# Performance work log

Measured on AMD Instinct MI355X. Metric: run time of the kernel, lower is better.

## Reference

```python
import jax, jax.numpy as jnp
import numpy as np

N_NODES = 20000
N_EDGES = 320000
IN_F = 256
OUT_F = 64
HEADS = 4
ALPHA = 0.1  # leaky_relu negative slope


def setup_inputs() -> dict:
    key = jax.random.key(0)
    ks = jax.random.split(key, 8)
    return {
        "input1": jax.random.normal(ks[0], (N_NODES, IN_F), jnp.float32),
        "input2": jax.random.normal(ks[1], (N_NODES, IN_F), jnp.float32),
        # per-head params: Ws maps source feats -> target_out, Wt maps target feats -> source_out
        "Ws": jax.random.normal(ks[2], (HEADS, IN_F, OUT_F), jnp.float32) * 0.06,
        "Wt": jax.random.normal(ks[3], (HEADS, IN_F, OUT_F), jnp.float32) * 0.06,
        "a1": jax.random.normal(ks[4], (HEADS, 2 * OUT_F), jnp.float32) * 0.1,
        "a2": jax.random.normal(ks[5], (HEADS, 2 * OUT_F), jnp.float32) * 0.1,
        # COO nonzeros of A_opt [n_target, n_source]
        "tgt_idx": jax.random.randint(ks[6], (N_EDGES,), 0, N_NODES),
        "src_idx": jax.random.randint(ks[7], (N_EDGES,), 0, N_NODES),
    }


def _segment_softmax(scores, seg, num_segments):
    m = jax.lax.stop_gradient(jax.ops.segment_max(scores, seg, num_segments=num_segments))
    w = jnp.exp(scores - m[seg])
    d = jax.ops.segment_sum(w, seg, num_segments=num_segments)
    d = jnp.where(d == 0, 1.0, d)
    return w / d[seg]


def _head(x1, x2, Ws, Wt, a1, a2, src, tgt, n_s, n_t):
    s = x1 @ Ws  # [n_s, OUT_F]  messages source -> target
    t = x2 @ Wt  # [n_t, OUT_F]  messages target -> source
    out = Ws.shape[1]
    # edge score e = leaky_relu(a^T [s_src || t_tgt]); split a to avoid edge-level concat
    e1 = jax.nn.leaky_relu((s @ a1[:out])[src] + (t @ a1[out:])[tgt], ALPHA)
    e2 = jax.nn.leaky_relu((s @ a2[:out])[src] + (t @ a2[out:])[tgt], ALPHA)
    alpha_ts = _segment_softmax(e1, tgt, n_t)  # softmax over sources per target
    alpha_st = _segment_softmax(e2, src, n_s)  # softmax over targets per source
    h_ts = jax.ops.segment_sum(alpha_ts[:, None] * s[src], tgt, num_segments=n_t)
    h_st = jax.ops.segment_sum(alpha_st[:, None] * t[tgt], src, num_segments=n_s)
    return jax.nn.elu(h_st), jax.nn.elu(h_ts)  # concat=True -> ELU per head


def reference(input1, input2, Ws, Wt, a1, a2, tgt_idx, src_idx):
    n_s, n_t = input1.shape[0], input2.shape[0]
    head_fn = jax.vmap(
        lambda W1, W2, v1, v2: _head(input1, input2, W1, W2, v1, v2, src_idx, tgt_idx, n_s, n_t)
    )
    h_st, h_ts = head_fn(Ws, Wt, a1, a2)  # each [H, n, OUT_F]
    h_st = jnp.transpose(h_st, (1, 0, 2)).reshape(n_s, -1)  # concat heads
    h_ts = jnp.transpose(h_ts, (1, 0, 2)).reshape(n_t, -1)
    return h_st, h_ts
```

## Files before the change

kernel.cpp:

```cpp
#include <hip/hip_runtime.h>
#include <math.h>

#define N_NODES 20000
#define N_EDGES 320000
#define IN_F 256
#define OUT_F 64
#define HEADS 4
#define NCOL 256
#define LRELU_ALPHA 0.1f
#define ELL_CAP 64

#define SCAT_X 313
#define GEMM_GB 157

typedef __attribute__((ext_vector_type(8))) short short8;
typedef __attribute__((ext_vector_type(4))) float floatx4;

__device__ __forceinline__ float lrelu(float x) {
    return x > 0.f ? x : LRELU_ALPHA * x;
}
__device__ __forceinline__ unsigned short f2bf(float f) {
    unsigned int u = __float_as_uint(f);
    u = (u + 0x7FFF + ((u >> 16) & 1)) >> 16;
    return (unsigned short)u;
}
__device__ __forceinline__ float bf2f(unsigned short u) {
    return __uint_as_float(((unsigned int)u) << 16);
}

__global__ __launch_bounds__(256) void prep_w_kernel(
    const float* __restrict__ Ws, const float* __restrict__ Wt,
    unsigned short* __restrict__ Wsb, unsigned short* __restrict__ Wtb,
    int* __restrict__ cnt)
{
    const int gid = blockIdx.x * 256 + threadIdx.x;

    for (int i = gid; i < 2 * N_NODES; i += 16384) cnt[i] = 0;

    const int mat = gid >> 13;
    const int r   = gid & 8191;
    const int kc  = r >> 8;
    const int c   = r & 255;
    const float* W    = mat ? Wt : Ws;
    unsigned short* O = mat ? Wtb : Wsb;
    const int h = c >> 6, j = c & 63;
    const int k0 = kc * 8;
    unsigned short v[8] __attribute__((aligned(16)));
#pragma unroll
    for (int i = 0; i < 8; ++i)
        v[i] = f2bf(W[(size_t)h * (IN_F * OUT_F) + (size_t)(k0 + i) * OUT_F + j]);
    *(uint4*)(O + (size_t)c * IN_F + k0) = *(const uint4*)v;
}

__global__ __launch_bounds__(512, 4) void hybrid_kernel(
    const float* __restrict__ A0, const unsigned short* __restrict__ Wb0,
    const float* __restrict__ A1, const unsigned short* __restrict__ Wb1,
    unsigned short* __restrict__ C0, unsigned short* __restrict__ C1,
    const float* __restrict__ a1, const float* __restrict__ a2,
    float* __restrict__ ss1, float* __restrict__ ss2,
    float* __restrict__ tt1, float* __restrict__ tt2,
    const int* __restrict__ src, const int* __restrict__ tgt,
    int* __restrict__ cnt_t, int* __restrict__ cnt_s,
    unsigned short* __restrict__ elist_t, unsigned short* __restrict__ elist_s)
{
    const int tid = threadIdx.x;

    __shared__ __align__(16) unsigned short Bl[128][264];

    if (blockIdx.x < SCAT_X) {
        const int e = ((int)blockIdx.y * SCAT_X + (int)blockIdx.x) * 512 + tid;
        if (e < N_EDGES) {
            const int s = src[e], t = tgt[e];
            const int p = atomicAdd(&cnt_t[t], 1);
            const int q = atomicAdd(&cnt_s[s], 1);
            if (p < ELL_CAP) elist_t[t * ELL_CAP + p] = (unsigned short)s;
            if (q < ELL_CAP) elist_s[s * ELL_CAP + q] = (unsigned short)t;
        }
        return;
    }

    const int gx   = blockIdx.x - SCAT_X;
    const int half = gx & 1;
    const int gb   = gx >> 1;
    const float* A           = (blockIdx.y == 0) ? A0 : A1;
    const unsigned short* Wb = (blockIdx.y == 0) ? Wb0 : Wb1;
    unsigned short* C        = (blockIdx.y == 0) ? C0 : C1;

    for (int i = tid; i < 4096; i += 512) {
        const int n  = i >> 5;
        const int kc = (i & 31) << 3;
        *(uint4*)&Bl[n][kc] = *(const uint4*)(Wb + (size_t)(half * 128 + n) * IN_F + kc);
    }
    __syncthreads();

    const int lane = tid & 63;
    const int w    = tid >> 6;
    const int quad = lane >> 4;
    const int l15  = lane & 15;
    const int g    = gb * 8 + w;
    if (g >= 1250) return;

    const float* arow = A + (size_t)(g * 16 + l15) * IN_F + quad * 8;

    float4 ua[8];
#pragma unroll
    for (int kk = 0; kk < 4; ++kk) {
        ua[2 * kk]     = *(const float4*)(arow + kk * 32);
        ua[2 * kk + 1] = *(const float4*)(arow + kk * 32 + 4);
    }
    short8 af[4];
#pragma unroll
    for (int kk = 0; kk < 4; ++kk) {
        short8 t;
        t[0] = (short)f2bf(ua[2 * kk].x);     t[1] = (short)f2bf(ua[2 * kk].y);
        t[2] = (short)f2bf(ua[2 * kk].z);     t[3] = (short)f2bf(ua[2 * kk].w);
        t[4] = (short)f2bf(ua[2 * kk + 1].x); t[5] = (short)f2bf(ua[2 * kk + 1].y);
        t[6] = (short)f2bf(ua[2 * kk + 1].z); t[7] = (short)f2bf(ua[2 * kk + 1].w);
        af[kk] = t;
    }

    float4 ub[8];
#pragma unroll
    for (int kk = 0; kk < 4; ++kk) {
        ub[2 * kk]     = *(const float4*)(arow + (kk + 4) * 32);
        ub[2 * kk + 1] = *(const float4*)(arow + (kk + 4) * 32 + 4);
    }

    floatx4 acc[8];
#pragma unroll
    for (int c = 0; c < 8; ++c) acc[c] = (floatx4){0.f, 0.f, 0.f, 0.f};

#pragma unroll
    for (int kk = 0; kk < 4; ++kk) {
#pragma unroll
        for (int c = 0; c < 8; ++c) {
            short8 bfrag = *(const short8*)&Bl[c * 16 + l15][kk * 32 + quad * 8];
            acc[c] = __builtin_amdgcn_mfma_f32_16x16x32_bf16(af[kk], bfrag, acc[c], 0, 0, 0);
        }
    }

#pragma unroll
    for (int kk = 0; kk < 4; ++kk) {
        short8 t;
        t[0] = (short)f2bf(ub[2 * kk].x);     t[1] = (short)f2bf(ub[2 * kk].y);
        t[2] = (short)f2bf(ub[2 * kk].z);     t[3] = (short)f2bf(ub[2 * kk].w);
        t[4] = (short)f2bf(ub[2 * kk + 1].x); t[5] = (short)f2bf(ub[2 * kk + 1].y);
        t[6] = (short)f2bf(ub[2 * kk + 1].z); t[7] = (short)f2bf(ub[2 * kk + 1].w);
        af[kk] = t;
    }
#pragma unroll
    for (int kk = 0; kk < 4; ++kk) {
#pragma unroll
        for (int c = 0; c < 8; ++c) {
            short8 bfrag = *(const short8*)&Bl[c * 16 + l15][(kk + 4) * 32 + quad * 8];
            acc[c] = __builtin_amdgcn_mfma_f32_16x16x32_bf16(af[kk], bfrag, acc[c], 0, 0, 0);
        }
    }

#pragma unroll
    for (int c = 0; c < 8; ++c) {
        const int col = half * 128 + c * 16 + l15;
#pragma unroll
        for (int r = 0; r < 4; ++r) {
            const int m = g * 16 + quad * 4 + r;
            C[(size_t)m * NCOL + col] = f2bf(acc[c][r]);
        }
    }

    const int off_aj = (blockIdx.y == 0) ? 0 : 64;
    float* o1 = (blockIdx.y == 0) ? ss1 : tt1;
    float* o2 = (blockIdx.y == 0) ? ss2 : tt2;

    float p1[2][4] = {{0.f,0.f,0.f,0.f},{0.f,0.f,0.f,0.f}};
    float p2[2][4] = {{0.f,0.f,0.f,0.f},{0.f,0.f,0.f,0.f}};
#pragma unroll
    for (int c = 0; c < 8; ++c) {
        const int hl = c >> 2;
        const int hh = half * 2 + hl;
        const int jj = (c & 3) * 16 + l15;
        const float w1 = a1[hh * 128 + off_aj + jj];
        const float w2 = a2[hh * 128 + off_aj + jj];
#pragma unroll
        for (int r = 0; r < 4; ++r) {
            p1[hl][r] += acc[c][r] * w1;
            p2[hl][r] += acc[c][r] * w2;
        }
    }
#pragma unroll
    for (int m = 1; m < 16; m <<= 1) {
#pragma unroll
        for (int hl = 0; hl < 2; ++hl)
#pragma unroll
            for (int r = 0; r < 4; ++r) {
                p1[hl][r] += __shfl_xor(p1[hl][r], m, 64);
                p2[hl][r] += __shfl_xor(p2[hl][r], m, 64);
            }
    }
    if (l15 == 0) {
#pragma unroll
        for (int r = 0; r < 4; ++r) {
            const int m = g * 16 + quad * 4 + r;
#pragma unroll
            for (int hl = 0; hl < 2; ++hl) {
                const int hh = half * 2 + hl;
                o1[m * HEADS + hh] = p1[hl][r];
                o2[m * HEADS + hh] = p2[hl][r];
            }
        }
    }
}

__global__ __launch_bounds__(256) void agg_kernel(
    const int* __restrict__ cnt_t, const unsigned short* __restrict__ elist_t,
    const int* __restrict__ cnt_s, const unsigned short* __restrict__ elist_s,
    const float* __restrict__ ss1, const float* __restrict__ ss2,
    const float* __restrict__ tt1, const float* __restrict__ tt2,
    const unsigned short* __restrict__ s_bf, const unsigned short* __restrict__ t_bf,
    float* __restrict__ h_st, float* __restrict__ h_ts)
{
    const int b    = blockIdx.x;
    const int dir  = b & 1;
    const int wave = threadIdx.x >> 6;
    const int lane = threadIdx.x & 63;
    const int n    = (b >> 1) * 4 + wave;
    const int h    = lane >> 4;
    const int coff = lane * 4;

    const int*            cnt   = dir ? cnt_s   : cnt_t;
    const unsigned short* list  = dir ? elist_s : elist_t;
    const unsigned short* table = dir ? t_bf    : s_bf;
    const float*          nsc   = dir ? ss2     : tt1;
    const float*          esc   = dir ? tt2     : ss1;
    float*                outp  = dir ? h_st    : h_ts;

    const float base = nsc[n * HEADS + h];
    int deg = cnt[n];
    if (deg > ELL_CAP) deg = ELL_CAP;
    const int b0 = n * ELL_CAP, b1 = b0 + deg;

    float4 acc = make_float4(0.f, 0.f, 0.f, 0.f);
    float den = 0.f;

    int p = b0;
    for (; p + 3 < b1; p += 4) {
        int m0 = list[p],     m1 = list[p + 1];
        int m2 = list[p + 2], m3 = list[p + 3];
        float e0 = esc[m0 * HEADS + h], e1 = esc[m1 * HEADS + h];
        float e2 = esc[m2 * HEADS + h], e3 = esc[m3 * HEADS + h];
        ushort4 r0 = *(const ushort4*)(table + (size_t)m0 * NCOL + coff);
        ushort4 r1 = *(const ushort4*)(table + (size_t)m1 * NCOL + coff);
        ushort4 r2 = *(const ushort4*)(table + (size_t)m2 * NCOL + coff);
        ushort4 r3 = *(const ushort4*)(table + (size_t)m3 * NCOL + coff);
        float w0 = __expf(lrelu(e0 + base));
        float w1 = __expf(lrelu(e1 + base));
        float w2 = __expf(lrelu(e2 + base));
        float w3 = __expf(lrelu(e3 + base));
        den += (w0 + w1) + (w2 + w3);
        acc.x += (w0 * bf2f(r0.x) + w1 * bf2f(r1.x)) + (w2 * bf2f(r2.x) + w3 * bf2f(r3.x));
        acc.y += (w0 * bf2f(r0.y) + w1 * bf2f(r1.y)) + (w2 * bf2f(r2.y) + w3 * bf2f(r3.y));
        acc.z += (w0 * bf2f(r0.z) + w1 * bf2f(r1.z)) + (w2 * bf2f(r2.z) + w3 * bf2f(r3.z));
        acc.w += (w0 * bf2f(r0.w) + w1 * bf2f(r1.w)) + (w2 * bf2f(r2.w) + w3 * bf2f(r3.w));
    }
    for (; p < b1; ++p) {
        int m0 = list[p];
        float w0 = __expf(lrelu(esc[m0 * HEADS + h] + base));
        ushort4 r0 = *(const ushort4*)(table + (size_t)m0 * NCOL + coff);
        den += w0;
        acc.x += w0 * bf2f(r0.x);
        acc.y += w0 * bf2f(r0.y);
        acc.z += w0 * bf2f(r0.z);
        acc.w += w0 * bf2f(r0.w);
    }

    if (den == 0.f) den = 1.f;
    float inv = 1.f / den;
    float4 r;
    r.x = acc.x * inv; r.y = acc.y * inv; r.z = acc.z * inv; r.w = acc.w * inv;
    r.x = (r.x > 0.f) ? r.x : expm1f(r.x);
    r.y = (r.y > 0.f) ? r.y : expm1f(r.y);
    r.z = (r.z > 0.f) ? r.z : expm1f(r.z);
    r.w = (r.w > 0.f) ? r.w : expm1f(r.w);
    *(float4*)(outp + (size_t)n * NCOL + coff) = r;
}

extern "C" void kernel_launch(void* const* d_in, const int* in_sizes, int n_in,
                              void* d_out, int out_size, void* d_ws, size_t ws_size,
                              hipStream_t stream)
{
    const float* input1 = (const float*)d_in[0];
    const float* input2 = (const float*)d_in[1];
    const float* Ws     = (const float*)d_in[2];
    const float* Wt     = (const float*)d_in[3];
    const float* a1     = (const float*)d_in[4];
    const float* a2     = (const float*)d_in[5];
    const int*   tgt    = (const int*)d_in[6];
    const int*   src    = (const int*)d_in[7];

    float* out  = (float*)d_out;
    float* h_st = out;
    float* h_ts = out + (size_t)N_NODES * NCOL;

    unsigned short* s_bf = (unsigned short*)d_ws;
    unsigned short* t_bf = s_bf + (size_t)N_NODES * NCOL;
    unsigned short* Wsb  = t_bf + (size_t)N_NODES * NCOL;
    unsigned short* Wtb  = Wsb + 256 * 256;
    float* ss1  = (float*)(Wtb + 256 * 256);
    float* ss2  = ss1 + N_NODES * HEADS;
    float* tt1  = ss2 + N_NODES * HEADS;
    float* tt2  = tt1 + N_NODES * HEADS;
    int*   cnt_t = (int*)(tt2 + N_NODES * HEADS);
    int*   cnt_s = cnt_t + N_NODES;
    unsigned short* elist_t = (unsigned short*)(cnt_s + N_NODES);
    unsigned short* elist_s = elist_t + (size_t)N_NODES * ELL_CAP;

    prep_w_kernel<<<64, 256, 0, stream>>>(Ws, Wt, Wsb, Wtb, cnt_t);

    dim3 ggrid(SCAT_X + GEMM_GB * 2, 2);
    hybrid_kernel<<<ggrid, 512, 0, stream>>>(input1, Wsb, input2, Wtb,
                                             s_bf, t_bf, a1, a2,
                                             ss1, ss2, tt1, tt2,
                                             src, tgt, cnt_t, cnt_s,
                                             elist_t, elist_s);

    agg_kernel<<<10000, 256, 0, stream>>>(cnt_t, elist_t, cnt_s, elist_s,
                                          ss1, ss2, tt1, tt2, s_bf, t_bf, h_st, h_ts);
}
```

Measured before the change: 184.5 us.

## Fuse weight prep, edge scatter, GEMM and aggregation into one cooperative kernel

Replaces the three kernel launches with a single cooperative persistent kernel of 512 blocks that uses grid-wide syncs between the phases: weight conversion and counter zeroing, then edge scatter plus the bf16 MFMA GEMM, then per-node softmax aggregation. This removes launch gaps and inter-kernel drains. In exchange, parallelism is capped at 512 blocks, each aggregation block walks a fixed node range with 8 waves, and grid.sync adds barrier cost. If the cooperative launch fails, the code falls back to the old three-kernel path.

After: 468.7 us. +154.0%, slower.

```diff
diff --git a/kernel.cpp b/kernel.cpp
--- a/kernel.cpp
+++ b/kernel.cpp
@@ -1,5 +1,8 @@
 #include <hip/hip_runtime.h>
+#include <hip/hip_cooperative_groups.h>
 #include <math.h>
+
+namespace cg = cooperative_groups;
 
 #define N_NODES 20000
 #define N_EDGES 320000
@@ -10,6 +13,9 @@
 #define LRELU_ALPHA 0.1f
 #define ELL_CAP 64
 
+#define FUSED_BLOCKS 512
+#define FUSED_THREADS 512
+
 #define SCAT_X 313
 #define GEMM_GB 157
 
@@ -26,6 +32,258 @@
 }
 __device__ __forceinline__ float bf2f(unsigned short u) {
     return __uint_as_float(((unsigned int)u) << 16);
+}
+
+__global__ __launch_bounds__(512, 4) void fused_kernel(
+    const float* __restrict__ A0, const float* __restrict__ A1,
+    const float* __restrict__ Ws, const float* __restrict__ Wt,
+    const float* __restrict__ a1, const float* __restrict__ a2,
+    const int* __restrict__ src, const int* __restrict__ tgt,
+    unsigned short* __restrict__ Wsb, unsigned short* __restrict__ Wtb,
+    unsigned short* __restrict__ C0, unsigned short* __restrict__ C1,
+    float* __restrict__ ss1, float* __restrict__ ss2,
+    float* __restrict__ tt1, float* __restrict__ tt2,
+    int* __restrict__ cnt_t, int* __restrict__ cnt_s,
+    unsigned short* __restrict__ elist_t, unsigned short* __restrict__ elist_s,
+    float* __restrict__ h_st, float* __restrict__ h_ts)
+{
+    cg::grid_group grid = cg::this_grid();
+    const int tid = threadIdx.x;
+    const int blk = blockIdx.x;
+    const int gid = blk * FUSED_THREADS + tid;
+
+    __shared__ __align__(16) unsigned short Bl[128][264];
+
+    if (gid < 2 * N_NODES) cnt_t[gid] = 0;
+    if (gid < 16384) {
+        const int mat = gid >> 13;
+        const int r   = gid & 8191;
+        const int kc  = r >> 8;
+        const int c   = r & 255;
+        const float* W    = mat ? Wt : Ws;
+        unsigned short* O = mat ? Wtb : Wsb;
+        const int h = c >> 6, j = c & 63;
+        const int k0 = kc * 8;
+        unsigned short v[8] __attribute__((aligned(16)));
+#pragma unroll
+        for (int i = 0; i < 8; ++i)
+            v[i] = f2bf(W[(size_t)h * (IN_F * OUT_F) + (size_t)(k0 + i) * OUT_F + j]);
+        *(uint4*)(O + (size_t)c * IN_F + k0) = *(const uint4*)v;
+    }
+
+    grid.sync();
+
+    for (int e = gid; e < N_EDGES; e += FUSED_BLOCKS * FUSED_THREADS) {
+        const int s = src[e], t = tgt[e];
+        const int p = atomicAdd(&cnt_t[t], 1);
+        const int q = atomicAdd(&cnt_s[s], 1);
+        if (p < ELL_CAP) elist_t[t * ELL_CAP + p] = (unsigned short)s;
+        if (q < ELL_CAP) elist_s[s * ELL_CAP + q] = (unsigned short)t;
+    }
+
+    {
+        const int y    = blk >> 8;
+        const int half = (blk >> 7) & 1;
+        const int bi   = blk & 127;
+        const float* A           = y ? A1 : A0;
+        const unsigned short* Wb = y ? Wtb : Wsb;
+        unsigned short* C        = y ? C1 : C0;
+
+        for (int i = tid; i < 4096; i += 512) {
+            const int n  = i >> 5;
+            const int kc = (i & 31) << 3;
+            *(uint4*)&Bl[n][kc] = *(const uint4*)(Wb + (size_t)(half * 128 + n) * IN_F + kc);
+        }
+        __syncthreads();
+
+        const int lane = tid & 63;
+        const int w    = tid >> 6;
+        const int quad = lane >> 4;
+        const int l15  = lane & 15;
+
+        const int off_aj = y ? 64 : 0;
+        float* o1 = y ? tt1 : ss1;
+        float* o2 = y ? tt2 : ss2;
+
+        for (int g = bi * 8 + w; g < 1250; g += 1024) {
+            const float* arow = A + (size_t)(g * 16 + l15) * IN_F + quad * 8;
+
+            float4 ua[8];
+#pragma unroll
+            for (int kk = 0; kk < 4; ++kk) {
+                ua[2 * kk]     = *(const float4*)(arow + kk * 32);
+                ua[2 * kk + 1] = *(const float4*)(arow + kk * 32 + 4);
+            }
+            short8 af[4];
+#pragma unroll
+            for (int kk = 0; kk < 4; ++kk) {
+                short8 t;
+                t[0] = (short)f2bf(ua[2 * kk].x);     t[1] = (short)f2bf(ua[2 * kk].y);
+                t[2] = (short)f2bf(ua[2 * kk].z);     t[3] = (short)f2bf(ua[2 * kk].w);
+                t[4] = (short)f2bf(ua[2 * kk + 1].x); t[5] = (short)f2bf(ua[2 * kk + 1].y);
+                t[6] = (short)f2bf(ua[2 * kk + 1].z); t[7] = (short)f2bf(ua[2 * kk + 1].w);
+                af[kk] = t;
+            }
+
+            float4 ub[8];
+#pragma unroll
+            for (int kk = 0; kk < 4; ++kk) {
+                ub[2 * kk]     = *(const float4*)(arow + (kk + 4) * 32);
+                ub[2 * kk + 1] = *(const float4*)(arow + (kk + 4) * 32 + 4);
+            }
+
+            floatx4 acc[8];
+#pragma unroll
+            for (int c = 0; c < 8; ++c) acc[c] = (floatx4){0.f, 0.f, 0.f, 0.f};
+
+#pragma unroll
+            for (int kk = 0; kk < 4; ++kk) {
+#pragma unroll
+                for (int c = 0; c < 8; ++c) {
+                    short8 bfrag = *(const short8*)&Bl[c * 16 + l15][kk * 32 + quad * 8];
+                    acc[c] = __builtin_amdgcn_mfma_f32_16x16x32_bf16(af[kk], bfrag, acc[c], 0, 0, 0);
+                }
+            }
+
+#pragma unroll
+            for (int kk = 0; kk < 4; ++kk) {
+                short8 t;
+                t[0] = (short)f2bf(ub[2 * kk].x);     t[1] = (short)f2bf(ub[2 * kk].y);
+                t[2] = (short)f2bf(ub[2 * kk].z);     t[3] = (short)f2bf(ub[2 * kk].w);
+                t[4] = (short)f2bf(ub[2 * kk + 1].x); t[5] = (short)f2bf(ub[2 * kk + 1].y);
+                t[6] = (short)f2bf(ub[2 * kk + 1].z); t[7] = (short)f2bf(ub[2 * kk + 1].w);
+                af[kk] = t;
+            }
+#pragma unroll
+            for (int kk = 0; kk < 4; ++kk) {
+#pragma unroll
+                for (int c = 0; c < 8; ++c) {
+                    short8 bfrag = *(const short8*)&Bl[c * 16 + l15][(kk + 4) * 32 + quad * 8];
+                    acc[c] = __builtin_amdgcn_mfma_f32_16x16x32_bf16(af[kk], bfrag, acc[c], 0, 0, 0);
+                }
+            }
+
+#pragma unroll
+            for (int c = 0; c < 8; ++c) {
+                const int col = half * 128 + c * 16 + l15;
+#pragma unroll
+                for (int r = 0; r < 4; ++r) {
+                    const int m = g * 16 + quad * 4 + r;
+                    C[(size_t)m * NCOL + col] = f2bf(acc[c][r]);
+                }
+            }
+
+            float p1[2][4] = {{0.f,0.f,0.f,0.f},{0.f,0.f,0.f,0.f}};
+            float p2[2][4] = {{0.f,0.f,0.f,0.f},{0.f,0.f,0.f,0.f}};
+#pragma unroll
+            for (int c = 0; c < 8; ++c) {
+                const int hl = c >> 2;
+                const int hh = half * 2 + hl;
+                const int jj = (c & 3) * 16 + l15;
+                const float w1 = a1[hh * 128 + off_aj + jj];
+                const float w2 = a2[hh * 128 + off_aj + jj];
+#pragma unroll
+                for (int r = 0; r < 4; ++r) {
+                    p1[hl][r] += acc[c][r] * w1;
+                    p2[hl][r] += acc[c][r] * w2;
+                }
+            }
+#pragma unroll
+            for (int m = 1; m < 16; m <<= 1) {
+#pragma unroll
+                for (int hl = 0; hl < 2; ++hl)
+#pragma unroll
+                    for (int r = 0; r < 4; ++r) {
+                        p1[hl][r] += __shfl_xor(p1[hl][r], m, 64);
+                        p2[hl][r] += __shfl_xor(p2[hl][r], m, 64);
+                    }
+            }
+            if (l15 == 0) {
+#pragma unroll
+                for (int r = 0; r < 4; ++r) {
+                    const int m = g * 16 + quad * 4 + r;
+#pragma unroll
+                    for (int hl = 0; hl < 2; ++hl) {
+                        const int hh = half * 2 + hl;
+                        o1[m * HEADS + hh] = p1[hl][r];
+                        o2[m * HEADS + hh] = p2[hl][r];
+                    }
+                }
+            }
+        }
+    }
+
+    grid.sync();
+
+    {
+        const int dir = blk & 1;
+        const int bi2 = blk >> 1;
+        const int wave = tid >> 6;
+        const int lane = tid & 63;
+        const int h    = lane >> 4;
+        const int coff = lane * 4;
+
+        const int*            cnt   = dir ? cnt_s   : cnt_t;
+        const unsigned short* list  = dir ? elist_s : elist_t;
+        const unsigned short* table = dir ? C1      : C0;
+        const float*          nsc   = dir ? ss2     : tt1;
+        const float*          esc   = dir ? tt2     : ss1;
+        float*                outp  = dir ? h_st    : h_ts;
+
+        const int nstart = (bi2 * N_NODES) >> 8;
+        const int nend   = ((bi2 + 1) * N_NODES) >> 8;
+
+        for (int n = nstart + wave; n < nend; n += 8) {
+            const float base = nsc[n * HEADS + h];
+            int deg = cnt[n];
+            if (deg > ELL_CAP) deg = ELL_CAP;
+            const int b0 = n * ELL_CAP, b1 = b0 + deg;
+
+            float4 acc = make_float4(0.f, 0.f, 0.f, 0.f);
+            float den = 0.f;
+
+            int p = b0;
+            for (; p + 3 < b1; p += 4) {
+                int m0 = list[p],     m1 = list[p + 1];
+                int m2 = list[p + 2], m3 = list[p + 3];
+                float e0 = esc[m0 * HEADS + h], e1 = esc[m1 * HEADS + h];
+                float e2 = esc[m2 * HEADS + h], e3 = esc[m3 * HEADS + h];
+                ushort4 r0 = *(const ushort4*)(table + (size_t)m0 * NCOL + coff);
+                ushort4 r1 = *(const ushort4*)(table + (size_t)m1 * NCOL + coff);
+                ushort4 r2 = *(const ushort4*)(table + (size_t)m2 * NCOL + coff);
+                ushort4 r3 = *(const ushort4*)(table + (size_t)m3 * NCOL + coff);
+                float w0 = __expf(lrelu(e0 + base));
+                float w1 = __expf(lrelu(e1 + base));
+                float w2 = __expf(lrelu(e2 + base));
+                float w3 = __expf(lrelu(e3 + base));
+                den += (w0 + w1) + (w2 + w3);
+                acc.x += (w0 * bf2f(r0.x) + w1 * bf2f(r1.x)) + (w2 * bf2f(r2.x) + w3 * bf2f(r3.x));
+                acc.y += (w0 * bf2f(r0.y) + w1 * bf2f(r1.y)) + (w2 * bf2f(r2.y) + w3 * bf2f(r3.y));
+                acc.z += (w0 * bf2f(r0.z) + w1 * bf2f(r1.z)) + (w2 * bf2f(r2.z) + w3 * bf2f(r3.z));
+                acc.w += (w0 * bf2f(r0.w) + w1 * bf2f(r1.w)) + (w2 * bf2f(r2.w) + w3 * bf2f(r3.w));
+            }
+            for (; p < b1; ++p) {
+                int m0 = list[p];
+                float w0 = __expf(lrelu(esc[m0 * HEADS + h] + base));
+                ushort4 r0 = *(const ushort4*)(table + (size_t)m0 * NCOL + coff);
+                den += w0;
+                acc.x += w0 * bf2f(r0.x);
+                acc.y += w0 * bf2f(r0.y);
+                acc.z += w0 * bf2f(r0.z);
+                acc.w += w0 * bf2f(r0.w);
+            }
+
+            if (den == 0.f) den = 1.f;
+            float inv = 1.f / den;
+            float4 r;
+            r.x = acc.x * inv; r.y = acc.y * inv; r.z = acc.z * inv; r.w = acc.w * inv;
+            r.x = (r.x > 0.f) ? r.x : expm1f(r.x);
+            r.y = (r.y > 0.f) ? r.y : expm1f(r.y);
+            r.z = (r.z > 0.f) ? r.z : expm1f(r.z);
+            r.w = (r.w > 0.f) ? r.w : expm1f(r.w);
+            *(float4*)(outp + (size_t)n * NCOL + coff) = r;
+        }
+    }
 }
 
 __global__ __launch_bounds__(256) void prep_w_kernel(
@@ -34,9 +292,7 @@
     int* __restrict__ cnt)
 {
     const int gid = blockIdx.x * 256 + threadIdx.x;
-
     for (int i = gid; i < 2 * N_NODES; i += 16384) cnt[i] = 0;
-
     const int mat = gid >> 13;
     const int r   = gid & 8191;
     const int kc  = r >> 8;
@@ -64,7 +320,6 @@
     unsigned short* __restrict__ elist_t, unsigned short* __restrict__ elist_s)
 {
     const int tid = threadIdx.x;
-
     __shared__ __align__(16) unsigned short Bl[128][264];
 
     if (blockIdx.x < SCAT_X) {
@@ -118,27 +373,22 @@
         t[6] = (short)f2bf(ua[2 * kk + 1].z); t[7] = (short)f2bf(ua[2 * kk + 1].w);
         af[kk] = t;
     }
-
     float4 ub[8];
 #pragma unroll
     for (int kk = 0; kk < 4; ++kk) {
         ub[2 * kk]     = *(const float4*)(arow + (kk + 4) * 32);
         ub[2 * kk + 1] = *(const float4*)(arow + (kk + 4) * 32 + 4);
     }
-
     floatx4 acc[8];
 #pragma unroll
     for (int c = 0; c < 8; ++c) acc[c] = (floatx4){0.f, 0.f, 0.f, 0.f};
-
-#pragma unroll
-    for (int kk = 0; kk < 4; ++kk) {
+#pragma unroll
+    for (int kk = 0; kk < 4; ++kk)
 #pragma unroll
         for (int c = 0; c < 8; ++c) {
             short8 bfrag = *(const short8*)&Bl[c * 16 + l15][kk * 32 + quad * 8];
             acc[c] = __builtin_amdgcn_mfma_f32_16x16x32_bf16(af[kk], bfrag, acc[c], 0, 0, 0);
         }
-    }
-
 #pragma unroll
     for (int kk = 0; kk < 4; ++kk) {
         short8 t;
@@ -149,14 +399,12 @@
         af[kk] = t;
     }
 #pragma unroll
-    for (int kk = 0; kk < 4; ++kk) {
+    for (int kk = 0; kk < 4; ++kk)
 #pragma unroll
         for (int c = 0; c < 8; ++c) {
             short8 bfrag = *(const short8*)&Bl[c * 16 + l15][(kk + 4) * 32 + quad * 8];
             acc[c] = __builtin_amdgcn_mfma_f32_16x16x32_bf16(af[kk], bfrag, acc[c], 0, 0, 0);
         }
-    }
-
 #pragma unroll
     for (int c = 0; c < 8; ++c) {
         const int col = half * 128 + c * 16 + l15;
@@ -166,11 +414,9 @@
             C[(size_t)m * NCOL + col] = f2bf(acc[c][r]);
         }
     }
-
     const int off_aj = (blockIdx.y == 0) ? 0 : 64;
     float* o1 = (blockIdx.y == 0) ? ss1 : tt1;
     float* o2 = (blockIdx.y == 0) ? ss2 : tt2;
-
     float p1[2][4] = {{0.f,0.f,0.f,0.f},{0.f,0.f,0.f,0.f}};
     float p2[2][4] = {{0.f,0.f,0.f,0.f},{0.f,0.f,0.f,0.f}};
 #pragma unroll
@@ -187,7 +433,7 @@
         }
     }
 #pragma unroll
-    for (int m = 1; m < 16; m <<= 1) {
+    for (int m = 1; m < 16; m <<= 1)
 #pragma unroll
         for (int hl = 0; hl < 2; ++hl)
 #pragma unroll
@@ -195,7 +441,6 @@
                 p1[hl][r] += __shfl_xor(p1[hl][r], m, 64);
                 p2[hl][r] += __shfl_xor(p2[hl][r], m, 64);
             }
-    }
     if (l15 == 0) {
 #pragma unroll
         for (int r = 0; r < 4; ++r) {
@@ -240,7 +485,6 @@
 
     float4 acc = make_float4(0.f, 0.f, 0.f, 0.f);
     float den = 0.f;
-
     int p = b0;
     for (; p + 3 < b1; p += 4) {
         int m0 = list[p],     m1 = list[p + 1];
@@ -271,7 +515,6 @@
         acc.z += w0 * bf2f(r0.z);
         acc.w += w0 * bf2f(r0.w);
     }
-
     if (den == 0.f) den = 1.f;
     float inv = 1.f / den;
     float4 r;
@@ -313,15 +556,28 @@
     unsigned short* elist_t = (unsigned short*)(cnt_s + N_NODES);
     unsigned short* elist_s = elist_t + (size_t)N_NODES * ELL_CAP;
 
-    prep_w_kernel<<<64, 256, 0, stream>>>(Ws, Wt, Wsb, Wtb, cnt_t);
-
-    dim3 ggrid(SCAT_X + GEMM_GB * 2, 2);
-    hybrid_kernel<<<ggrid, 512, 0, stream>>>(input1, Wsb, input2, Wtb,
-                                             s_bf, t_bf, a1, a2,
-                                             ss1, ss2, tt1, tt2,
-                                             src, tgt, cnt_t, cnt_s,
-                                             elist_t, elist_s);
-
-    agg_kernel<<<10000, 256, 0, stream>>>(cnt_t, elist_t, cnt_s, elist_s,
-                                          ss1, ss2, tt1, tt2, s_bf, t_bf, h_st, h_ts);
-}
+    void* args[] = {
+        (void*)&input1, (void*)&input2, (void*)&Ws, (void*)&Wt,
+        (void*)&a1, (void*)&a2, (void*)&src, (void*)&tgt,
+        (void*)&Wsb, (void*)&Wtb, (void*)&s_bf, (void*)&t_bf,
+        (void*)&ss1, (void*)&ss2, (void*)&tt1, (void*)&tt2,
+        (void*)&cnt_t, (void*)&cnt_s, (void*)&elist_t, (void*)&elist_s,
+        (void*)&h_st, (void*)&h_ts
+    };
+    hipError_t err = hipLaunchCooperativeKernel(
+        (const void*)fused_kernel, dim3(FUSED_BLOCKS), dim3(FUSED_THREADS),
+        args, 0, stream);
+
+    if (err != hipSuccess) {
+        prep_w_kernel<<<64, 256, 0, stream>>>(Ws, Wt, Wsb, Wtb, cnt_t);
+        dim3 ggrid(SCAT_X + GEMM_GB * 2, 2);
+        hybrid_kernel<<<ggrid, 512, 0, stream>>>(input1, Wsb, input2, Wtb,
+                                                 s_bf, t_bf, a1, a2,
+                                                 ss1, ss2, tt1, tt2,
+                                                 src, tgt, cnt_t, cnt_s,
+                                                 elist_t, elist_s);
+        agg_kernel<<<10000, 256, 0, stream>>>(cnt_t, elist_t, cnt_s, elist_s,
+                                              ss1, ss2, tt1, tt2, s_bf, t_bf,
+                                              h_st, h_ts);
+    }
+}
```
